# Performance work log

Hardware: AMD Instinct MI355X
Metric: run time of the kernel (lower is better)

Reference implementation:

```python
import jax, jax.numpy as jnp
import numpy as np

EPS = 1e-8


def setup_inputs() -> dict:
    key = jax.random.key(0)
    ks = jax.random.split(key, 8)
    B, N, D = 8, 2048, 768
    H, R = 768, 4
    return {
        "x": jax.random.normal(ks[0], (B, N, D), dtype=jnp.float32),
        "scale": jnp.ones((D,), dtype=jnp.float32),
        "U": jax.random.normal(ks[1], (H, R), dtype=jnp.float32) * 0.02,
        "V": jax.random.normal(ks[2], (H, R), dtype=jnp.float32) * 0.02,
        "S_param": jax.random.normal(ks[3], (H, H), dtype=jnp.float32) * 0.01,
        "Bm": jax.random.normal(ks[4], (H, D), dtype=jnp.float32) * (1.0 / np.sqrt(D)),
        "Cm": jax.random.normal(ks[5], (D, H), dtype=jnp.float32) * (1.0 / np.sqrt(H)),
        "gate_w": jax.random.normal(ks[6], (D, D), dtype=jnp.float32) * (1.0 / np.sqrt(D)),
        "gate_b": jnp.zeros((D,), dtype=jnp.float32),
        "alpha": jnp.full((1,), 0.1, dtype=jnp.float32),
    }


def reference(x, scale, U, V, S_param, Bm, Cm, gate_w, gate_b, alpha):
    B, N, D = x.shape
    H = Bm.shape[0]
    # A = diag(A_diag) + U V^T + (S - S^T); A_diag is a fixed buffer.
    A_diag = -jnp.linspace(1.0, float(H), H, dtype=x.dtype) / H
    A = jnp.diag(A_diag) + U @ V.T + (S_param - S_param.T)
    At = A.T  # apply as h @ A.T
    # RMSNorm
    rms = jnp.sqrt(jnp.mean(x * x, axis=-1, keepdims=True) + EPS)
    xn = x / rms * scale
    # Precompute input injections u_t = x_t @ B.T for all t: (N, B, H)
    u = jnp.einsum('bnd,hd->nbh', xn, Bm)

    def step(h, ut):
        h = h @ At + ut
        return h, h @ Cm.T  # (B, D)

    h0 = jnp.zeros((B, H), dtype=x.dtype)
    _, y_fwd = jax.lax.scan(step, h0, u)                 # (N, B, D)
    _, y_bwd = jax.lax.scan(step, h0, u, reverse=True)   # (N, B, D), indexed in time order
    y = 0.5 * (y_fwd + y_bwd)
    y = jnp.swapaxes(y, 0, 1)  # (B, N, D)
    # Gate
    g = jax.nn.sigmoid(jnp.einsum('bnd,ed->bne', xn, gate_w) + gate_b)
    y = y * g
    # Skip (dropout is identity in eval)
    return x + alpha * y
```

## Files before the change

kernel.cpp:

```cpp
#include <hip/hip_runtime.h>


typedef short  bfrag __attribute__((ext_vector_type(8)));
typedef float  ffrag __attribute__((ext_vector_type(4)));
typedef float  f4    __attribute__((ext_vector_type(4)));
typedef short  s4v   __attribute__((ext_vector_type(4)));

#define DEV static __device__ __forceinline__
#define Hn 768
#define FLS 132
#define BLS 260

DEV unsigned short f2bf(float f) {
  unsigned u = __float_as_uint(f);
  u += 0x7fffu + ((u >> 16) & 1u);
  return (unsigned short)(u >> 16);
}
DEV float bf2f(unsigned short s) { return __uint_as_float(((unsigned)s) << 16); }

DEV ffrag mfma16(bfrag a, bfrag b, ffrag c) {
  return __builtin_amdgcn_mfma_f32_16x16x32_bf16(a, b, c, 0, 0, 0);
}

DEV void glds16(const unsigned short* g, unsigned short* l) {
  __builtin_amdgcn_global_load_lds(
      (const __attribute__((address_space(1))) unsigned int*)g,
      (__attribute__((address_space(3))) unsigned int*)l, 16, 0, 0);
}

template<int N> DEV void vwait() {
  if constexpr (N == 0)      asm volatile("s_waitcnt vmcnt(0)" ::: "memory");
  else if constexpr (N == 4) asm volatile("s_waitcnt vmcnt(4)" ::: "memory");
}

union BF8 { bfrag v; unsigned short u[8]; };

__global__ __launch_bounds__(256) void k_abuild(
    const float* __restrict__ U, const float* __restrict__ V,
    const float* __restrict__ S, const float* __restrict__ Bm,
    const float* __restrict__ Cm, const float* __restrict__ gw,
    float* __restrict__ Af, float* __restrict__ AfT,
    unsigned short* __restrict__ Abf,
    unsigned short* __restrict__ Bmb, unsigned short* __restrict__ Cmb,
    unsigned short* __restrict__ gwb, unsigned short* __restrict__ zp) {
  int i = blockIdx.x;
  int task = blockIdx.y;
  if (task == 0) {
    float u0 = U[i*4+0], u1 = U[i*4+1], u2 = U[i*4+2], u3 = U[i*4+3];
    for (int j = threadIdx.x; j < Hn; j += 256) {
      float a = u0*V[j*4+0] + u1*V[j*4+1] + u2*V[j*4+2] + u3*V[j*4+3]
              + S[i*Hn+j] - S[j*Hn+i];
      if (i == j) a += -(float)(i+1) / 768.0f;
      Af[i*Hn+j]  = a;
      AfT[j*Hn+i] = a;
      Abf[i*Hn+j] = f2bf(a);
    }
    if (i == 0) for (int j = threadIdx.x; j < 1024; j += 256) zp[j] = 0;
  } else {
    const float* src = (task==1) ? Bm : (task==2) ? Cm : gw;
    unsigned short* dst = (task==1) ? Bmb : (task==2) ? Cmb : gwb;
    for (int j = threadIdx.x; j < Hn; j += 256) dst[i*Hn+j] = f2bf(src[i*Hn+j]);
  }
}

__global__ __launch_bounds__(256) void k_rms(
    const float* __restrict__ x, const float* __restrict__ scale,
    unsigned short* __restrict__ xn) {
  int row  = blockIdx.x * 4 + (threadIdx.x >> 6);
  int lane = threadIdx.x & 63;
  int b = row >> 11, t = row & 2047;
  const float* xr = x + (long)row * Hn;
  float v[12];
  float ss = 0.f;
#pragma unroll
  for (int j = 0; j < 12; ++j) { v[j] = xr[lane + j*64]; ss += v[j]*v[j]; }
#pragma unroll
  for (int off = 1; off < 64; off <<= 1) ss += __shfl_xor(ss, off);
  float inv = 1.0f / sqrtf(ss / 768.0f + 1e-8f);
  unsigned short* dst = xn + ((long)t * 8 + b) * Hn;
#pragma unroll
  for (int j = 0; j < 12; ++j) dst[lane + j*64] = f2bf(v[j] * inv * scale[lane + j*64]);
}

__global__ __launch_bounds__(512) void k_sq(
    const float* __restrict__ X, const float* __restrict__ XT,
    float* __restrict__ Z, float* __restrict__ ZT,
    unsigned short* __restrict__ Zbf) {
  int tid = threadIdx.x, lane = tid & 63, w = tid >> 6;
  int mw = w >> 2, nw = w & 3, l15 = lane & 15, lhi = lane >> 4;
  int rb = blockIdx.x * 64, cb = blockIdx.y * 128;
  ffrag acc[2][2] = {};
  for (int kt = 0; kt < 24; ++kt) {
    int k0 = kt*32 + lhi*8;
    BF8 ah[2], al[2], bh[2], bl[2];
#pragma unroll
    for (int mt = 0; mt < 2; ++mt) {
      const f4* p = (const f4*)(X + (long)(rb + mw*32 + mt*16 + l15) * Hn + k0);
      f4 x0 = p[0], x1 = p[1];
#pragma unroll
      for (int j = 0; j < 8; ++j) {
        float f = (j < 4) ? x0[j] : x1[j-4];
        unsigned short h = f2bf(f);
        ah[mt].u[j] = h; al[mt].u[j] = f2bf(f - bf2f(h));
      }
    }
#pragma unroll
    for (int nt = 0; nt < 2; ++nt) {
      const f4* p = (const f4*)(XT + (long)(cb + nw*32 + nt*16 + l15) * Hn + k0);
      f4 x0 = p[0], x1 = p[1];
#pragma unroll
      for (int j = 0; j < 8; ++j) {
        float f = (j < 4) ? x0[j] : x1[j-4];
        unsigned short h = f2bf(f);
        bh[nt].u[j] = h; bl[nt].u[j] = f2bf(f - bf2f(h));
      }
    }
#pragma unroll
    for (int mt = 0; mt < 2; ++mt)
#pragma unroll
      for (int nt = 0; nt < 2; ++nt) {
        acc[mt][nt] = mfma16(ah[mt].v, bh[nt].v, acc[mt][nt]);
        acc[mt][nt] = mfma16(ah[mt].v, bl[nt].v, acc[mt][nt]);
        acc[mt][nt] = mfma16(al[mt].v, bh[nt].v, acc[mt][nt]);
      }
  }
#pragma unroll
  for (int mt = 0; mt < 2; ++mt)
#pragma unroll
    for (int nt = 0; nt < 2; ++nt)
#pragma unroll
      for (int q = 0; q < 4; ++q) {
        int grow = rb + mw*32 + mt*16 + lhi*4 + q;
        int gcol = cb + nw*32 + nt*16 + l15;
        float vv = acc[mt][nt][q];
        Z[(long)grow*Hn + gcol] = vv;
        ZT[(long)gcol*Hn + grow] = vv;
        Zbf[(long)grow*Hn + gcol] = f2bf(vv);
      }
}

__global__ __launch_bounds__(512) void k_lvl256(
    const unsigned short* __restrict__ A0s, const unsigned short* __restrict__ B0s,
    const unsigned short* __restrict__ res, unsigned short* __restrict__ outb,
    const unsigned short* __restrict__ zp, int sh) {
  __shared__ __align__(16) unsigned short ldsb[3 * 16384];

  const int tid = threadIdx.x, lane = tid & 63, w = tid >> 6;
  const int l15 = lane & 15, lhi = lane >> 4;
  const int wr = w >> 2, wc = w & 3;

  const int nwg = gridDim.x;
  const int q8 = nwg >> 3, r8 = nwg & 7, xcd = blockIdx.x & 7, fo = blockIdx.x >> 3;
  const int wg = (xcd < r8 ? xcd*(q8+1) : r8*(q8+1) + (xcd - r8)*q8) + fo;
  const int cb = wg % 3, rbk = wg / 3;
  const long r0  = (long)rbk * 256;
  const long bc0 = (long)cb * 256;
  const int dir = (r0 >= 16384) ? 1 : 0;

  const bool skip = dir ? (r0 >= 32768 - sh) : (r0 + 256 <= sh);

  const int rowin = lane >> 2, ch = lane & 3;
  long gA[2]; bool vA[2]; long gB[2]; int lbase[2];
#pragma unroll
  for (int j = 0; j < 2; ++j) {
    const int rl = j*128 + w*16 + rowin;
    const int c = ch ^ ((rl ^ (rl >> 2)) & 3);
    lbase[j] = j*4096 + w*512;
    long gr = r0 + rl + (dir ? sh : -sh);
    vA[j] = dir ? (gr < 32768) : (gr >= 0);
    gA[j] = gr * Hn + c*8;
    gB[j] = (bc0 + rl) * Hn + c*8;
  }

  auto stage = [&](int buf, int kt) {
    const int ko = kt * 32;
    unsigned short* dst = ldsb + buf * 16384;
#pragma unroll
    for (int j = 0; j < 2; ++j) {
      const unsigned short* g = vA[j] ? (A0s + gA[j] + ko) : zp;
      glds16(g, dst + lbase[j]);
      glds16(B0s + gB[j] + ko, dst + 8192 + lbase[j]);
    }
  };

  ffrag acc[8][4] = {};
  const int cx = (lhi ^ ((l15 ^ (l15 >> 2)) & 3)) * 8;

  if (!skip) {
    stage(0, 0); stage(1, 1);
    for (int kt = 0; kt < 24; ++kt) {
      if (kt < 23) vwait<4>(); else vwait<0>();
      __builtin_amdgcn_s_barrier();
      if (kt + 2 <= 23) stage((kt + 2) % 3, kt + 2);
      const unsigned short* L = ldsb + (kt % 3) * 16384;
      bfrag b[4];
#pragma unroll
      for (int nt = 0; nt < 4; ++nt)
        b[nt] = *(const bfrag*)&L[8192 + (wc*64 + nt*16 + l15)*32 + cx];
#pragma unroll
      for (int mh = 0; mh < 2; ++mh) {
        bfrag a[4];
#pragma unroll
        for (int m4 = 0; m4 < 4; ++m4)
          a[m4] = *(const bfrag*)&L[(wr*128 + (mh*4 + m4)*16 + l15)*32 + cx];
#pragma unroll
        for (int m4 = 0; m4 < 4; ++m4)
#pragma unroll
          for (int nt = 0; nt < 4; ++nt)
            acc[mh*4 + m4][nt] = mfma16(a[m4], b[nt], acc[mh*4 + m4][nt]);
      }
    }
  }

  float* fl = (float*)ldsb;
#pragma unroll
  for (int p = 0; p < 8; ++p) {
    __syncthreads();
#pragma unroll
    for (int nt = 0; nt < 4; ++nt)
#pragma unroll
      for (int q = 0; q < 4; ++q)
        fl[(wr*16 + lhi*4 + q)*BLS + wc*64 + nt*16 + l15] = acc[p][nt][q];
    __syncthreads();
    for (int i = tid; i < 2048; i += 512) {
      const int srow = i >> 6;
      const int cc   = (i & 63) << 2;
      f4 v = *(const f4*)&fl[srow*BLS + cc];
      const long grow = r0 + (srow >> 4)*128 + p*16 + (srow & 15);
      const long gcol = bc0 + cc;
      const long go = grow * Hn + gcol;
      s4v rv = *(const s4v*)&res[go];
#pragma unroll
      for (int j = 0; j < 4; ++j) v[j] += bf2f(((unsigned short*)&rv)[j]);
      s4v ov;
#pragma unroll
      for (int j = 0; j < 4; ++j) ((unsigned short*)&ov)[j] = f2bf(v[j]);
      *(s4v*)&outb[go] = ov;
    }
  }
}

__global__ __launch_bounds__(512) void k_cmb(
    const unsigned short* __restrict__ A0s, const unsigned short* __restrict__ B0s,
    const unsigned short* __restrict__ res, unsigned short* __restrict__ outb,
    const unsigned short* __restrict__ zp, int sh) {
  constexpr int BUFS = 2 * 4096 + 8192;
  __shared__ __align__(16) unsigned short ldsb[2 * BUFS];

  const int tid = threadIdx.x, lane = tid & 63, w = tid >> 6;
  const int l15 = lane & 15, lhi = lane >> 4;
  const int wr = w >> 2, wc = w & 3;

  const int nwg = gridDim.x;
  const int q8 = nwg >> 3, r8 = nwg & 7, xcd = blockIdx.x & 7, fo = blockIdx.x >> 3;
  const int wg = (xcd < r8 ? xcd*(q8+1) : r8*(q8+1) + (xcd - r8)*q8) + fo;
  const int cb = wg % 3, rbk = wg / 3;
  const long r0  = (long)rbk * 128;
  const long bc0 = (long)cb * 256;

  const int rowin = lane >> 2, ch = lane & 3;
  const int rA = w*16 + rowin;
  const int cswz = ch ^ ((rowin ^ (rowin >> 2)) & 3);
  long gA[2]; bool vA[2];
  { long g0 = r0 + rA - sh;         vA[0] = (g0 >= 0);    gA[0] = g0 * Hn + cswz*8; }
  { long g1 = r0 + rA + 16384 + sh; vA[1] = (g1 < 32768); gA[1] = g1 * Hn + cswz*8; }
  long gB[2];
#pragma unroll
  for (int j = 0; j < 2; ++j)
    gB[j] = (bc0 + j*128 + rA) * Hn + cswz*8;

  auto stage = [&](int buf, int kt) {
    const int ko = kt * 32;
    unsigned short* dst = ldsb + buf * BUFS;
#pragma unroll
    for (int s = 0; s < 2; ++s) {
      const unsigned short* g = vA[s] ? (A0s + gA[s] + ko) : zp;
      glds16(g, dst + s*4096 + w*512);
    }
#pragma unroll
    for (int j = 0; j < 2; ++j)
      glds16(B0s + gB[j] + ko, dst + 2*4096 + j*4096 + w*512);
  };

  ffrag acc[4][4] = {};
  const int cx = (lhi ^ ((l15 ^ (l15 >> 2)) & 3)) * 8;

  stage(0, 0);
  __syncthreads();
  int cur = 0;
  for (int kt = 0; kt < 24; ++kt) {
    if (kt < 23) stage(cur ^ 1, kt + 1);
    const unsigned short* L = ldsb + cur * BUFS;
    bfrag a[2][4], b[4];
#pragma unroll
    for (int mt = 0; mt < 4; ++mt) {
      const int row = wr*64 + mt*16 + l15;
      a[0][mt] = *(const bfrag*)&L[row*32 + cx];
      a[1][mt] = *(const bfrag*)&L[4096 + row*32 + cx];
    }
#pragma unroll
    for (int nt = 0; nt < 4; ++nt) {
      const int row = wc*64 + nt*16 + l15;
      b[nt] = *(const bfrag*)&L[2*4096 + row*32 + cx];
    }
#pragma unroll
    for (int mt = 0; mt < 4; ++mt)
#pragma unroll
      for (int nt = 0; nt < 4; ++nt) {
        acc[mt][nt] = mfma16(a[0][mt], b[nt], acc[mt][nt]);
        acc[mt][nt] = mfma16(a[1][mt], b[nt], acc[mt][nt]);
      }
    __syncthreads();
    cur ^= 1;
  }

  float* fl = (float*)ldsb;
#pragma unroll
  for (int p = 0; p < 4; ++p) {
    __syncthreads();
#pragma unroll
    for (int nt = 0; nt < 4; ++nt)
#pragma unroll
      for (int q = 0; q < 4; ++q)
        fl[(wr*16 + lhi*4 + q)*BLS + wc*64 + nt*16 + l15] = acc[p][nt][q];
    __syncthreads();
    for (int i = tid; i < 2048; i += 512) {
      const int srow = i >> 6;
      const int cc   = (i & 63) << 2;
      f4 v = *(const f4*)&fl[srow*BLS + cc];
      const long grow = r0 + (srow >> 4)*64 + p*16 + (srow & 15);
      const long gcol = bc0 + cc;
      const long go = grow * Hn + gcol;
      s4v ra = *(const s4v*)&res[go];
      s4v rb2 = *(const s4v*)&res[go + (long)16384*Hn];
#pragma unroll
      for (int j = 0; j < 4; ++j)
        v[j] += bf2f(((unsigned short*)&ra)[j]) + bf2f(((unsigned short*)&rb2)[j]);
      s4v ov;
#pragma unroll
      for (int j = 0; j < 4; ++j) ((unsigned short*)&ov)[j] = f2bf(v[j]);
      *(s4v*)&outb[go] = ov;
    }
  }
}

__global__ __launch_bounds__(256) void k_uz(
    const unsigned short* __restrict__ xn, const unsigned short* __restrict__ Bmb,
    const unsigned short* __restrict__ gwb,
    unsigned short* __restrict__ u, unsigned short* __restrict__ z) {
  __shared__ __align__(16) unsigned short ldsb[2 * 3 * 4096];

  const int tid = threadIdx.x, lane = tid & 63, w = tid >> 6;
  const int l15 = lane & 15, lhi = lane >> 4;
  const int wr = w >> 1, wc = w & 1;

  const int nwg = gridDim.x;
  const int q8 = nwg >> 3, r8 = nwg & 7, xcd = blockIdx.x & 7, fo = blockIdx.x >> 3;
  const int wg = (xcd < r8 ? xcd*(q8+1) : r8*(q8+1) + (xcd - r8)*q8) + fo;
  const int cb = wg % 6, rbk = wg / 6;
  const long r0 = (long)rbk * 128;
  const long bc0 = (long)cb * 128;

  const int rowin = lane >> 2, ch = lane & 3;
  long gA[2]; long gB[2]; int lbase[2];
#pragma unroll
  for (int jj = 0; jj < 2; ++jj) {
    const int inst = w*2 + jj;
    const int r = inst*16 + rowin;
    const int c = ch ^ ((r ^ (r >> 2)) & 3);
    lbase[jj] = inst * 512;
    gA[jj] = (r0 + r) * Hn + c*8;
    gB[jj] = (bc0 + r) * Hn + c*8;
  }

  auto stage = [&](int buf, int kt) {
    const int ko = kt * 32;
    unsigned short* dst = ldsb + buf * 12288;
#pragma unroll
    for (int jj = 0; jj < 2; ++jj) {
      glds16(xn  + gA[jj] + ko, dst + 0*4096 + lbase[jj]);
      glds16(Bmb + gB[jj] + ko, dst + 1*4096 + lbase[jj]);
      glds16(gwb + gB[jj] + ko, dst + 2*4096 + lbase[jj]);
    }
  };

  ffrag acc[4][4] = {};
  ffrag accZ[4][4] = {};
  const int cx = (lhi ^ ((l15 ^ (l15 >> 2)) & 3)) * 8;

  stage(0, 0);
  __syncthreads();
  int cur = 0;
  for (int kt = 0; kt < 24; ++kt) {
    if (kt < 23) stage(cur ^ 1, kt + 1);
    const unsigned short* L = ldsb + cur * 12288;
    bfrag a[4], b0[4], b1[4];
#pragma unroll
    for (int mt = 0; mt < 4; ++mt)
      a[mt] = *(const bfrag*)&L[(wr*64 + mt*16 + l15)*32 + cx];
#pragma unroll
    for (int nt = 0; nt < 4; ++nt) {
      const int row = wc*64 + nt*16 + l15;
      b0[nt] = *(const bfrag*)&L[1*4096 + row*32 + cx];
      b1[nt] = *(const bfrag*)&L[2*4096 + row*32 + cx];
    }
#pragma unroll
    for (int mt = 0; mt < 4; ++mt)
#pragma unroll
      for (int nt = 0; nt < 4; ++nt) {
        acc[mt][nt]  = mfma16(a[mt], b0[nt], acc[mt][nt]);
        accZ[mt][nt] = mfma16(a[mt], b1[nt], accZ[mt][nt]);
      }
    __syncthreads();
    cur ^= 1;
  }

  float* fl = (float*)ldsb;
#pragma unroll
  for (int which = 0; which < 2; ++which) {
#pragma unroll
    for (int hh = 0; hh < 2; ++hh) {
      __syncthreads();
      if (wr == hh) {
#pragma unroll
        for (int mt = 0; mt < 4; ++mt)
#pragma unroll
          for (int nt = 0; nt < 4; ++nt)
#pragma unroll
            for (int q = 0; q < 4; ++q)
              fl[(mt*16 + lhi*4 + q)*FLS + wc*64 + nt*16 + l15] =
                  which ? accZ[mt][nt][q] : acc[mt][nt][q];
      }
      __syncthreads();
      for (int i = tid; i < 2048; i += 256) {
        const int row = i >> 5;
        const int cc  = (i & 31) << 2;
        f4 v = *(const f4*)&fl[row*FLS + cc];
        const long go = (r0 + hh*64 + row) * Hn + bc0 + cc;
        s4v ov;
#pragma unroll
        for (int j = 0; j < 4; ++j) ((unsigned short*)&ov)[j] = f2bf(v[j]);
        if (which == 0) {
          *(s4v*)&u[go] = ov;
          *(s4v*)&u[go + (long)16384*Hn] = ov;
        } else {
          *(s4v*)&z[go] = ov;
        }
      }
    }
  }
}

__global__ __launch_bounds__(256) void k_fin2(
    const unsigned short* __restrict__ A0s, const unsigned short* __restrict__ B0s,
    const unsigned short* __restrict__ z,
    const float* __restrict__ gb, const float* __restrict__ alpha,
    const float* __restrict__ x, float* __restrict__ outf) {
  __shared__ __align__(16) char smem[34048];
  unsigned short* ldsb = (unsigned short*)smem;

  const int tid = threadIdx.x, lane = tid & 63, w = tid >> 6;
  const int l15 = lane & 15, lhi = lane >> 4;
  const int wr = w >> 1, wc = w & 1;

  const int nwg = gridDim.x;
  const int q8 = nwg >> 3, r8 = nwg & 7, xcd = blockIdx.x & 7, fo = blockIdx.x >> 3;
  const int wg = (xcd < r8 ? xcd*(q8+1) : r8*(q8+1) + (xcd - r8)*q8) + fo;
  const int cb = wg % 6, rbk = wg / 6;
  const long r0 = (long)rbk * 128;
  const long bc0 = (long)cb * 128;

  const int rowin = lane >> 2, ch = lane & 3;
  long gA[2]; long gB[2]; int lbase[2];
#pragma unroll
  for (int jj = 0; jj < 2; ++jj) {
    const int inst = w*2 + jj;
    const int r = inst*16 + rowin;
    const int c = ch ^ ((r ^ (r >> 2)) & 3);
    lbase[jj] = inst * 512;
    gA[jj] = (r0 + r) * Hn + c*8;
    gB[jj] = (bc0 + r) * Hn + c*8;
  }

  auto stage = [&](int buf, int kt) {
    const int ko = kt * 32;
    unsigned short* dst = ldsb + buf * 8192;
#pragma unroll
    for (int jj = 0; jj < 2; ++jj) {
      glds16(A0s + gA[jj] + ko, dst + lbase[jj]);
      glds16(B0s + gB[jj] + ko, dst + 4096 + lbase[jj]);
    }
  };

  ffrag acc[4][4] = {};
  const int cx = (lhi ^ ((l15 ^ (l15 >> 2)) & 3)) * 8;

  stage(0, 0);
  __syncthreads();
  int cur = 0;
  for (int kt = 0; kt < 24; ++kt) {
    if (kt < 23) stage(cur ^ 1, kt + 1);
    const unsigned short* L = ldsb + cur * 8192;
    bfrag a[4], b[4];
#pragma unroll
    for (int mt = 0; mt < 4; ++mt)
      a[mt] = *(const bfrag*)&L[(wr*64 + mt*16 + l15)*32 + cx];
#pragma unroll
    for (int nt = 0; nt < 4; ++nt)
      b[nt] = *(const bfrag*)&L[4096 + (wc*64 + nt*16 + l15)*32 + cx];
#pragma unroll
    for (int mt = 0; mt < 4; ++mt)
#pragma unroll
      for (int nt = 0; nt < 4; ++nt)
        acc[mt][nt] = mfma16(a[mt], b[nt], acc[mt][nt]);
    __syncthreads();
    cur ^= 1;
  }

  const float al = alpha[0];
  float* fl = (float*)smem;
#pragma unroll
  for (int hh = 0; hh < 2; ++hh) {
    __syncthreads();
    if (wr == hh) {
#pragma unroll
      for (int mt = 0; mt < 4; ++mt)
#pragma unroll
        for (int nt = 0; nt < 4; ++nt)
#pragma unroll
          for (int q = 0; q < 4; ++q)
            fl[(mt*16 + lhi*4 + q)*FLS + wc*64 + nt*16 + l15] = acc[mt][nt][q];
    }
    __syncthreads();
    for (int i = tid; i < 2048; i += 256) {
      const int row = i >> 5;
      const int cc  = (i & 31) << 2;
      f4 v = *(const f4*)&fl[row*FLS + cc];
      const long grow = r0 + hh*64 + row;
      const long gcol = bc0 + cc;
      const long go = grow * Hn + gcol;
      s4v zv = *(const s4v*)&z[go];
      f4 gbv = *(const f4*)&gb[gcol];
      const long t = grow >> 3, b = grow & 7;
      const long o = (b*2048 + t)*Hn + gcol;
      f4 xv = *(const f4*)&x[o];
      f4 ov;
#pragma unroll
      for (int j = 0; j < 4; ++j) {
        float zz = bf2f(((unsigned short*)&zv)[j]) + gbv[j];
        float g = 1.0f / (1.0f + __expf(-zz));
        ov[j] = xv[j] + al * 0.5f * v[j] * g;
      }
      *(f4*)&outf[o] = ov;
    }
  }
}

extern "C" void kernel_launch(void* const* d_in, const int* in_sizes, int n_in,
                              void* d_out, int out_size, void* d_ws, size_t ws_size,
                              hipStream_t stream) {
  const float* x     = (const float*)d_in[0];
  const float* scale = (const float*)d_in[1];
  const float* U     = (const float*)d_in[2];
  const float* V     = (const float*)d_in[3];
  const float* S     = (const float*)d_in[4];
  const float* Bm    = (const float*)d_in[5];
  const float* Cm    = (const float*)d_in[6];
  const float* gw    = (const float*)d_in[7];
  const float* gb    = (const float*)d_in[8];
  const float* alpha = (const float*)d_in[9];
  float* out = (float*)d_out;

  char* p = (char*)d_ws;
  auto alloc = [&](size_t sz) { char* r = p; p += (sz + 255) & ~(size_t)255; return r; };

  const size_t SZ_X  = (size_t)32768 * Hn * sizeof(unsigned short);
  const size_t SZ_BF = (size_t)16384 * Hn * sizeof(unsigned short);
  const size_t SZ_M  = (size_t)Hn * Hn * sizeof(float);
  const size_t SZ_MB = (size_t)Hn * Hn * sizeof(unsigned short);

  unsigned short* xn   = (unsigned short*)alloc(SZ_BF);
  unsigned short* zbuf = (unsigned short*)alloc(SZ_BF);
  unsigned short* XA = (unsigned short*)alloc(SZ_X);
  unsigned short* XB = (unsigned short*)alloc(SZ_X);
  float* Af  = (float*)alloc(SZ_M);
  float* AfT = (float*)alloc(SZ_M);
  float* P1  = (float*)alloc(SZ_M);
  float* P1T = (float*)alloc(SZ_M);
  float* P2  = (float*)alloc(SZ_M);
  float* P2T = (float*)alloc(SZ_M);
  unsigned short* Abf = (unsigned short*)alloc(SZ_MB);
  unsigned short* Ab[10];
  for (int i = 0; i < 10; ++i) Ab[i] = (unsigned short*)alloc(SZ_MB);
  unsigned short* Bmb = (unsigned short*)alloc(SZ_MB);
  unsigned short* Cmb = (unsigned short*)alloc(SZ_MB);
  unsigned short* gwb = (unsigned short*)alloc(SZ_MB);
  unsigned short* zp  = (unsigned short*)alloc(1024 * sizeof(unsigned short));

  if ((size_t)(p - (char*)d_ws) > ws_size) return;

  k_abuild<<<dim3(768, 4), 256, 0, stream>>>(U, V, S, Bm, Cm, gw,
      Af, AfT, Abf, Bmb, Cmb, gwb, zp);
  k_rms<<<4096, 256, 0, stream>>>(x, scale, xn);

  const float* sx = Af; const float* sxt = AfT;
  float* za = P1; float* zat = P1T; float* zb = P2; float* zbt = P2T;
  for (int i = 0; i < 10; ++i) {
    k_sq<<<dim3(12, 6), 512, 0, stream>>>(sx, sxt, za, zat, Ab[i]);
    sx = za; sxt = zat;
    float* t1 = za; float* t2 = zat; za = zb; zat = zbt; zb = t1; zbt = t2;
  }

  k_uz<<<768, 256, 0, stream>>>(xn, Bmb, gwb, XA, zbuf);

  unsigned short* src = XA; unsigned short* dst = XB;
  for (int i = 0; i < 10; ++i) {
    const unsigned short* W = (i == 0) ? Abf : Ab[i-1];
    k_lvl256<<<384, 512, 0, stream>>>(src, W, src, dst, zp, 8 << i);
    unsigned short* t = src; src = dst; dst = t;
  }
  k_cmb<<<384, 512, 0, stream>>>(src, Ab[9], src, XB, zp, 8192);

  k_fin2<<<768, 256, 0, stream>>>(XB, Cmb, zbuf, gb, alpha, x, out);
}
```

Baseline: 1.375 ms.

## Shrink level GEMM tile to 128x256 with 256 threads and double buffering

The per-level scan GEMM kernel moves from a 256x256 tile with 512 threads and a triple-buffered async pipeline to a 128x256 tile with 256 threads and a simple double buffer synchronized by __syncthreads. The grid doubles to 768 blocks, which gives finer granularity for the skipped-row regions and more blocks per GPU. In exchange, each tile reuses data less, and the prefetch pipeline is shallower, relying on barriers instead of vmcnt waits.

```diff
diff --git a/kernel.cpp b/kernel.cpp
--- a/kernel.cpp
+++ b/kernel.cpp
@@ -26,11 +26,6 @@
   __builtin_amdgcn_global_load_lds(
       (const __attribute__((address_space(1))) unsigned int*)g,
       (__attribute__((address_space(3))) unsigned int*)l, 16, 0, 0);
-}
-
-template<int N> DEV void vwait() {
-  if constexpr (N == 0)      asm volatile("s_waitcnt vmcnt(0)" ::: "memory");
-  else if constexpr (N == 4) asm volatile("s_waitcnt vmcnt(4)" ::: "memory");
 }
 
 union BF8 { bfrag v; unsigned short u[8]; };
@@ -139,94 +134,100 @@
       }
 }
 
-__global__ __launch_bounds__(512) void k_lvl256(
+__global__ __launch_bounds__(256) void k_lvl(
     const unsigned short* __restrict__ A0s, const unsigned short* __restrict__ B0s,
     const unsigned short* __restrict__ res, unsigned short* __restrict__ outb,
     const unsigned short* __restrict__ zp, int sh) {
-  __shared__ __align__(16) unsigned short ldsb[3 * 16384];
+  constexpr int BUFS = 4096 + 8192;
+  __shared__ __align__(16) unsigned short ldsb[2 * BUFS];
 
   const int tid = threadIdx.x, lane = tid & 63, w = tid >> 6;
   const int l15 = lane & 15, lhi = lane >> 4;
-  const int wr = w >> 2, wc = w & 3;
+  const int wr = w >> 1, wc = w & 1;
 
   const int nwg = gridDim.x;
   const int q8 = nwg >> 3, r8 = nwg & 7, xcd = blockIdx.x & 7, fo = blockIdx.x >> 3;
   const int wg = (xcd < r8 ? xcd*(q8+1) : r8*(q8+1) + (xcd - r8)*q8) + fo;
   const int cb = wg % 3, rbk = wg / 3;
-  const long r0  = (long)rbk * 256;
+  const long r0  = (long)rbk * 128;
   const long bc0 = (long)cb * 256;
   const int dir = (r0 >= 16384) ? 1 : 0;
-
-  const bool skip = dir ? (r0 >= 32768 - sh) : (r0 + 256 <= sh);
+  const bool skip = dir ? (r0 >= 32768 - sh) : (r0 + 128 <= sh);
 
   const int rowin = lane >> 2, ch = lane & 3;
-  long gA[2]; bool vA[2]; long gB[2]; int lbase[2];
-#pragma unroll
-  for (int j = 0; j < 2; ++j) {
-    const int rl = j*128 + w*16 + rowin;
-    const int c = ch ^ ((rl ^ (rl >> 2)) & 3);
-    lbase[j] = j*4096 + w*512;
+  const int cswz = ch ^ ((rowin ^ (rowin >> 2)) & 3);
+  long gA[2]; bool vA[2]; int lA[2];
+#pragma unroll
+  for (int jj = 0; jj < 2; ++jj) {
+    const int rl = (w*2 + jj)*16 + rowin;
     long gr = r0 + rl + (dir ? sh : -sh);
-    vA[j] = dir ? (gr < 32768) : (gr >= 0);
-    gA[j] = gr * Hn + c*8;
-    gB[j] = (bc0 + rl) * Hn + c*8;
+    vA[jj] = dir ? (gr < 32768) : (gr >= 0);
+    gA[jj] = gr * Hn + cswz*8;
+    lA[jj] = (w*2 + jj) * 512;
+  }
+  long gB[4]; int lB[4];
+#pragma unroll
+  for (int jj = 0; jj < 4; ++jj) {
+    const int rl = (w*4 + jj)*16 + rowin;
+    gB[jj] = (bc0 + rl) * Hn + cswz*8;
+    lB[jj] = 4096 + (w*4 + jj) * 512;
   }
 
   auto stage = [&](int buf, int kt) {
     const int ko = kt * 32;
-    unsigned short* dst = ldsb + buf * 16384;
-#pragma unroll
-    for (int j = 0; j < 2; ++j) {
-      const unsigned short* g = vA[j] ? (A0s + gA[j] + ko) : zp;
-      glds16(g, dst + lbase[j]);
-      glds16(B0s + gB[j] + ko, dst + 8192 + lbase[j]);
-    }
+    unsigned short* dst = ldsb + buf * BUFS;
+#pragma unroll
+    for (int jj = 0; jj < 2; ++jj) {
+      const unsigned short* g = vA[jj] ? (A0s + gA[jj] + ko) : zp;
+      glds16(g, dst + lA[jj]);
+    }
+#pragma unroll
+    for (int jj = 0; jj < 4; ++jj)
+      glds16(B0s + gB[jj] + ko, dst + lB[jj]);
   };
 
-  ffrag acc[8][4] = {};
+  ffrag acc[4][8] = {};
   const int cx = (lhi ^ ((l15 ^ (l15 >> 2)) & 3)) * 8;
 
   if (!skip) {
-    stage(0, 0); stage(1, 1);
+    stage(0, 0);
+    __syncthreads();
+    int cur = 0;
     for (int kt = 0; kt < 24; ++kt) {
-      if (kt < 23) vwait<4>(); else vwait<0>();
-      __builtin_amdgcn_s_barrier();
-      if (kt + 2 <= 23) stage((kt + 2) % 3, kt + 2);
-      const unsigned short* L = ldsb + (kt % 3) * 16384;
-      bfrag b[4];
-#pragma unroll
-      for (int nt = 0; nt < 4; ++nt)
-        b[nt] = *(const bfrag*)&L[8192 + (wc*64 + nt*16 + l15)*32 + cx];
-#pragma unroll
-      for (int mh = 0; mh < 2; ++mh) {
-        bfrag a[4];
-#pragma unroll
-        for (int m4 = 0; m4 < 4; ++m4)
-          a[m4] = *(const bfrag*)&L[(wr*128 + (mh*4 + m4)*16 + l15)*32 + cx];
-#pragma unroll
-        for (int m4 = 0; m4 < 4; ++m4)
-#pragma unroll
-          for (int nt = 0; nt < 4; ++nt)
-            acc[mh*4 + m4][nt] = mfma16(a[m4], b[nt], acc[mh*4 + m4][nt]);
-      }
+      if (kt < 23) stage(cur ^ 1, kt + 1);
+      const unsigned short* L = ldsb + cur * BUFS;
+      bfrag a[4], b[8];
+#pragma unroll
+      for (int mt = 0; mt < 4; ++mt)
+        a[mt] = *(const bfrag*)&L[(wr*64 + mt*16 + l15)*32 + cx];
+#pragma unroll
+      for (int nt = 0; nt < 8; ++nt)
+        b[nt] = *(const bfrag*)&L[4096 + (wc*128 + nt*16 + l15)*32 + cx];
+#pragma unroll
+      for (int mt = 0; mt < 4; ++mt)
+#pragma unroll
+        for (int nt = 0; nt < 8; ++nt)
+          acc[mt][nt] = mfma16(a[mt], b[nt], acc[mt][nt]);
+      __syncthreads();
+      cur ^= 1;
     }
   }
 
   float* fl = (float*)ldsb;
 #pragma unroll
-  for (int p = 0; p < 8; ++p) {
-    __syncthreads();
-#pragma unroll
-    for (int nt = 0; nt < 4; ++nt)
+  for (int p = 0; p < 4; ++p) {
+    __syncthreads();
+#pragma unroll
+    for (int nt = 0; nt < 8; ++nt)
 #pragma unroll
       for (int q = 0; q < 4; ++q)
-        fl[(wr*16 + lhi*4 + q)*BLS + wc*64 + nt*16 + l15] = acc[p][nt][q];
-    __syncthreads();
-    for (int i = tid; i < 2048; i += 512) {
+        fl[(wr*16 + lhi*4 + q)*BLS + wc*128 + nt*16 + l15] = acc[p][nt][q];
+    __syncthreads();
+    for (int i = tid; i < 2048; i += 256) {
       const int srow = i >> 6;
       const int cc   = (i & 63) << 2;
       f4 v = *(const f4*)&fl[srow*BLS + cc];
-      const long grow = r0 + (srow >> 4)*128 + p*16 + (srow & 15);
+      const long grow = r0 + (srow >> 4)*64 + p*16 + (srow & 15);
       const long gcol = bc0 + cc;
       const long go = grow * Hn + gcol;
       s4v rv = *(const s4v*)&res[go];
@@ -616,7 +617,7 @@
   unsigned short* src = XA; unsigned short* dst = XB;
   for (int i = 0; i < 10; ++i) {
     const unsigned short* W = (i == 0) ? Abf : Ab[i-1];
-    k_lvl256<<<384, 512, 0, stream>>>(src, W, src, dst, zp, 8 << i);
+    k_lvl<<<768, 256, 0, stream>>>(src, W, src, dst, zp, 8 << i);
     unsigned short* t = src; src = dst; dst = t;
   }
   k_cmb<<<384, 512, 0, stream>>>(src, Ab[9], src, XB, zp, 8192);
```

After: 1.636 ms. 19.0% more time.
